# Kernel optimization log

Measured on AMD Instinct MI355X. Metric: run time of the kernel, lower is better.

Reference implementation:

```python
import jax, jax.numpy as jnp
import numpy as np

N_TOKENS = 32768
DIM = 4096
N_EXPERTS = 64
TOPK = 2
UPDATE_BIAS_RATE = 0.001
ROUTE_SCALE = 1.0


def setup_inputs() -> dict:
    key = jax.random.key(0)
    k1, k2 = jax.random.split(key)
    x = jax.random.normal(k1, (N_TOKENS, DIM), dtype=jnp.float32)
    # gate projection weight, as in nn.Parameter(torch.empty(E, dim)) + kaiming init
    weight = jax.random.normal(k2, (N_EXPERTS, DIM), dtype=jnp.float32) * 0.02
    bias = jnp.zeros((N_EXPERTS,), dtype=jnp.float32)          # registered buffer
    target_dist = jnp.full((N_EXPERTS,), 1.0 / N_EXPERTS, dtype=jnp.float32)
    return {"x": x, "weight": weight, "bias": bias, "target_dist": target_dist}


def reference(x, weight, bias, target_dist):
    # scores = linear(nan_to_num(x), W) + bias, softmax in fp32
    xc = jnp.nan_to_num(x, nan=0.0)
    scores = (xc @ weight.T + bias).astype(jnp.float32)        # [N, E]
    probs = jax.nn.softmax(scores, axis=-1)                    # [N, E]
    # top-k: gathered values equal the top-k probabilities
    topv, indices = jax.lax.top_k(probs, TOPK)                 # [N, K], [N, K]
    weights = topv / jnp.sum(topv, axis=-1, keepdims=True)
    weights = weights * ROUTE_SCALE
    # load-balancing stats: bincount with float weights == segment_sum
    expert_weights_sum = jax.ops.segment_sum(
        weights.reshape(-1), indices.reshape(-1), num_segments=N_EXPERTS)
    total_weights = expert_weights_sum.sum()
    load_error = target_dist * total_weights - expert_weights_sum
    new_bias = bias + UPDATE_BIAS_RATE * (load_error / total_weights)
    return weights.astype(x.dtype), indices, new_bias
```

## Files before the change

### kernel.cpp

```cpp
#include <hip/hip_runtime.h>
#include <math.h>

#define N_TOKENS 32768
#define DIM      4096
#define NE       64
#define TM       64
#define BK       128
#define KHALF    (DIM / 2)
#define NBLK_MAIN (N_TOKENS / TM * 2)
#define NBLK_POST (N_TOKENS / 256)
#define EPS_GAP  2e-3f
#define REFINE_BLOCKS 1024

#define WOFF     65664
#define WL_OFF   16384
#define PART_OFF 128
#define PSC_OFF  524288
#define WFRAG_ELEMS (512 * 512)

typedef __bf16 bf16x4 __attribute__((ext_vector_type(4)));
typedef __bf16 bf16x8 __attribute__((ext_vector_type(8)));
typedef float  f32x16 __attribute__((ext_vector_type(16)));

__global__ __launch_bounds__(256) void prep_w(
    const float* __restrict__ w, float* __restrict__ ws)
{
    __bf16* whi = (__bf16*)(ws + WOFF);
    __bf16* wlo = whi + WFRAG_ELEMS;
    const int tid  = blockIdx.x * 256 + threadIdx.x;
    const int f    = tid >> 6, lane = tid & 63;
    const int nt   = f & 1,    K16  = f >> 1;
    const int e    = nt * 32 + (lane & 31);
    const int k    = K16 * 16 + (lane >> 5) * 8;
    const float4 a = *(const float4*)(w + (size_t)e * DIM + k);
    const float4 b = *(const float4*)(w + (size_t)e * DIM + k + 4);
    const float v[8] = {a.x, a.y, a.z, a.w, b.x, b.y, b.z, b.w};
    bf16x8 h, l;
    #pragma unroll
    for (int i = 0; i < 8; ++i) {
        h[i] = (__bf16)v[i];
        l[i] = (__bf16)(v[i] - (float)h[i]);
    }
    *(bf16x8*)(whi + (size_t)tid * 8) = h;
    *(bf16x8*)(wlo + (size_t)tid * 8) = l;
}

__device__ __forceinline__ void cvt_split(const float4 v, bf16x4& h, bf16x4& l) {
    h[0] = (__bf16)v.x; l[0] = (__bf16)(v.x - (float)h[0]);
    h[1] = (__bf16)v.y; l[1] = (__bf16)(v.y - (float)h[1]);
    h[2] = (__bf16)v.z; l[2] = (__bf16)(v.z - (float)h[2]);
    h[3] = (__bf16)v.w; l[3] = (__bf16)(v.w - (float)h[3]);
}

__global__ __launch_bounds__(256, 4) void gate_main(
    const float* __restrict__ x,
    float* __restrict__ ws)
{
    __shared__ __align__(16) unsigned char smem[32768];

    const __bf16* whi = (const __bf16*)(ws + WOFF);
    const __bf16* wlo = whi + WFRAG_ELEMS;
    float*        psc = ws + PSC_OFF;

    const int t    = threadIdx.x;
    const int lane = t & 63;
    const int wave = t >> 6;
    const int mt   = wave >> 1;
    const int nt   = wave & 1;
    const int kh   = blockIdx.x & 1;
    const int tb   = (blockIdx.x >> 1) * TM;
    const int kbeg = kh * KHALF;

    const int q     = t & 31;
    const int rbase = t >> 5;

    f32x16 acc0, acc12;
    #pragma unroll
    for (int i = 0; i < 16; ++i) { acc0[i] = 0.f; acc12[i] = 0.f; }

    float4 xv[8];
    #pragma unroll
    for (int j = 0; j < 8; ++j)
        xv[j] = *(const float4*)(x + (size_t)(tb + rbase + 8 * j) * DIM + kbeg + q * 4);

    const int tok0  = mt * 32 + (lane & 31);
    const int klane = lane >> 5;
    const int abase = tok0 * 256;
    const int aswz  = (tok0 & 7) << 4;

    for (int kc = kbeg; kc < kbeg + KHALF; kc += BK) {
        #pragma unroll
        for (int j = 0; j < 8; ++j) {
            const int r = rbase + 8 * j;
            bf16x4 h, l;
            cvt_split(xv[j], h, l);
            const int off = r * 256 + ((q * 8) ^ ((r & 7) << 4));
            *(bf16x4*)(&smem[off])         = h;
            *(bf16x4*)(&smem[16384 + off]) = l;
        }
        __syncthreads();

        if (kc + BK < kbeg + KHALF) {
            #pragma unroll
            for (int j = 0; j < 8; ++j)
                xv[j] = *(const float4*)(x + (size_t)(tb + rbase + 8 * j) * DIM + kc + BK + q * 4);
        }

        const int K16c = kc >> 4;
        #pragma unroll
        for (int ks = 0; ks < 8; ++ks) {
            const int aoff = abase + ((ks * 32 + klane * 16) ^ aswz);
            const bf16x8 ah = *(const bf16x8*)(&smem[aoff]);
            const bf16x8 al = *(const bf16x8*)(&smem[16384 + aoff]);
            const size_t bidx = ((size_t)((K16c + ks) * 2 + nt) * 64 + lane) * 8;
            const bf16x8 bh = *(const bf16x8*)(whi + bidx);
            const bf16x8 bl = *(const bf16x8*)(wlo + bidx);
            acc0  = __builtin_amdgcn_mfma_f32_32x32x16_bf16(ah, bh, acc0,  0, 0, 0);
            acc12 = __builtin_amdgcn_mfma_f32_32x32x16_bf16(al, bh, acc12, 0, 0, 0);
            acc12 = __builtin_amdgcn_mfma_f32_32x32x16_bf16(ah, bl, acc12, 0, 0, 0);
        }
        __syncthreads();
    }

    const int e = nt * 32 + (lane & 31);
    float* base = psc + (size_t)kh * N_TOKENS * NE;
    #pragma unroll
    for (int r = 0; r < 16; ++r) {
        const int tok = mt * 32 + (r & 3) + 8 * (r >> 2) + 4 * (lane >> 5);
        base[(size_t)(tb + tok) * NE + e] = acc0[r] + acc12[r];
    }
}

__global__ __launch_bounds__(256) void gate_post(
    const float* __restrict__ bias,
    float* __restrict__ out,
    float* __restrict__ ws)
{
    __shared__ float sbias[NE];
    __shared__ float part[NE];
    unsigned* wl_count = (unsigned*)(ws + 64);
    float*    partials = ws + PART_OFF;
    int*      wl       = (int*)(ws + WL_OFF);
    const float* psc   = ws + PSC_OFF;

    const int t = threadIdx.x;
    if (t < NE) { sbias[t] = bias[t]; part[t] = 0.f; }
    __syncthreads();

    const int tok = blockIdx.x * 256 + t;
    const float* p0 = psc + (size_t)tok * NE;
    const float* p1 = psc + (size_t)N_TOKENS * NE + (size_t)tok * NE;

    float v1 = -3e38f, v2 = -3e38f, v3 = -3e38f;
    int   i1 = 0,      i2 = 0;
    #pragma unroll
    for (int g = 0; g < 16; ++g) {
        const float4 a = *(const float4*)(p0 + g * 4);
        const float4 b = *(const float4*)(p1 + g * 4);
        float s[4] = {a.x + b.x, a.y + b.y, a.z + b.z, a.w + b.w};
        #pragma unroll
        for (int j = 0; j < 4; ++j) {
            const float sv = s[j] + sbias[g * 4 + j];
            const int   e  = g * 4 + j;
            if (sv > v1)      { v3 = v2; v2 = v1; i2 = i1; v1 = sv; i1 = e; }
            else if (sv > v2) { v3 = v2; v2 = sv; i2 = e; }
            else if (sv > v3) { v3 = sv; }
        }
    }
    const bool risky = (v1 - v2 < EPS_GAP) || (v2 - v3 < EPS_GAP);
    if (risky) {
        const int pos = (int)atomicAdd(wl_count, 1u);
        wl[pos] = tok;
    } else {
        const float ex = expf(v2 - v1);
        const float w1 = 1.f / (1.f + ex);
        const float w2 = ex * w1;
        const size_t g = (size_t)tok * 2;
        *(float2*)(out + g)                        = make_float2(w1, w2);
        *(float2*)(out + (size_t)N_TOKENS * 2 + g) = make_float2((float)i1, (float)i2);
        atomicAdd(&part[i1], w1);
        atomicAdd(&part[i2], w2);
    }
    __syncthreads();
    if (t < NE) partials[(size_t)blockIdx.x * NE + t] = part[t];
}

__global__ __launch_bounds__(256) void gate_refine(
    const float* __restrict__ x,
    const float* __restrict__ w,
    const float* __restrict__ bias,
    float* __restrict__ out,
    float* __restrict__ ws)
{
    float*          ews_ref  = ws;
    const unsigned* wl_count = (const unsigned*)(ws + 64);
    const int*      wl       = (const int*)(ws + WL_OFF);

    const int t = threadIdx.x;
    const int e = t >> 2;
    const int q = t & 3;
    __shared__ double sc[NE];

    const unsigned count = *wl_count;
    for (unsigned it = blockIdx.x; it < count; it += gridDim.x) {
        const int tok = wl[it];
        const float* xr = x + (size_t)tok * DIM;
        const float* wr = w + (size_t)e * DIM;
        double s = 0.0;
        const int k0 = q * (DIM / 4), k1 = k0 + DIM / 4;
        for (int k = k0; k < k1; k += 4) {
            const float4 a = *(const float4*)(xr + k);
            const float4 b = *(const float4*)(wr + k);
            s += (double)a.x * (double)b.x;
            s += (double)a.y * (double)b.y;
            s += (double)a.z * (double)b.z;
            s += (double)a.w * (double)b.w;
        }
        s += __shfl_xor(s, 1);
        s += __shfl_xor(s, 2);
        if (q == 0) sc[e] = s + (double)bias[e];
        __syncthreads();

        if (t == 0) {
            double v1 = -1e300, v2 = -1e300;
            int i1 = 0, i2 = 0;
            for (int j = 0; j < NE; ++j) {
                const double sv = sc[j];
                if (sv > v1)      { v2 = v1; i2 = i1; v1 = sv; i1 = j; }
                else if (sv > v2) { v2 = sv; i2 = j; }
            }
            const double ex = exp(v2 - v1);
            const double w1 = 1.0 / (1.0 + ex);
            const double w2 = ex * w1;
            const size_t g = (size_t)tok * 2;
            *(float2*)(out + g)                        = make_float2((float)w1, (float)w2);
            *(float2*)(out + (size_t)N_TOKENS * 2 + g) = make_float2((float)i1, (float)i2);
            atomicAdd(&ews_ref[i1], (float)w1);
            atomicAdd(&ews_ref[i2], (float)w2);
        }
        __syncthreads();
    }
}

__global__ void gate_bias(
    const float* __restrict__ bias,
    const float* __restrict__ target,
    const float* __restrict__ ws,
    float* __restrict__ out)
{
    const int e = threadIdx.x;
    const float* partials = ws + PART_OFF;
    float v = ws[e];
    for (int b = 0; b < NBLK_POST; ++b) v += partials[(size_t)b * NE + e];
    float total = v;
    #pragma unroll
    for (int off = 32; off > 0; off >>= 1)
        total += __shfl_xor(total, off);
    const float nb = bias[e] + 0.001f * ((target[e] * total - v) / total);
    out[(size_t)N_TOKENS * 4 + e] = nb;
}

extern "C" void kernel_launch(void* const* d_in, const int* in_sizes, int n_in,
                              void* d_out, int out_size, void* d_ws, size_t ws_size,
                              hipStream_t stream) {
    const float* x      = (const float*)d_in[0];
    const float* w      = (const float*)d_in[1];
    const float* bias   = (const float*)d_in[2];
    const float* target = (const float*)d_in[3];
    float* out = (float*)d_out;
    float* ws  = (float*)d_ws;

    hipMemsetAsync(ws, 0, 128 * sizeof(float), stream);
    prep_w     <<<128, 256, 0, stream>>>(w, ws);
    gate_main  <<<NBLK_MAIN, 256, 0, stream>>>(x, ws);
    gate_post  <<<NBLK_POST, 256, 0, stream>>>(bias, out, ws);
    gate_refine<<<REFINE_BLOCKS, 256, 0, stream>>>(x, w, bias, out, ws);
    gate_bias  <<<1, 64, 0, stream>>>(bias, target, ws, out);
}
```

Measured before the change: 281.4 us.

## Restructure gate GEMM into per-wave K-quarter split without LDS staging

The main gate kernel now gives each wave a quarter of the K dimension for a 32-token tile and loads x straight into registers, dropping the shared-memory staging and both barriers. The fp32 to bf16 hi/lo split is done with bit masking (truncation) instead of rounding conversions, and B fragments are double-buffered in registers. Partial scores are written as four K-quarter planes that the post kernel now sums, which doubles partial-score traffic. Each wave covers all 64 experts, so the x hi/lo fragments are reused across two accumulators, but register pressure rises and truncation slightly changes the split error.

```diff
diff --git a/kernel.cpp b/kernel.cpp
--- a/kernel.cpp
+++ b/kernel.cpp
@@ -4,10 +4,9 @@
 #define N_TOKENS 32768
 #define DIM      4096
 #define NE       64
-#define TM       64
-#define BK       128
-#define KHALF    (DIM / 2)
-#define NBLK_MAIN (N_TOKENS / TM * 2)
+#define KQ       4
+#define KSPAN    (DIM / KQ)
+#define NBLK_MAIN (N_TOKENS / 32)
 #define NBLK_POST (N_TOKENS / 256)
 #define EPS_GAP  2e-3f
 #define REFINE_BLOCKS 1024
@@ -18,7 +17,6 @@
 #define PSC_OFF  524288
 #define WFRAG_ELEMS (512 * 512)
 
-typedef __bf16 bf16x4 __attribute__((ext_vector_type(4)));
 typedef __bf16 bf16x8 __attribute__((ext_vector_type(8)));
 typedef float  f32x16 __attribute__((ext_vector_type(16)));
 
@@ -35,99 +33,134 @@
     const float4 a = *(const float4*)(w + (size_t)e * DIM + k);
     const float4 b = *(const float4*)(w + (size_t)e * DIM + k + 4);
     const float v[8] = {a.x, a.y, a.z, a.w, b.x, b.y, b.z, b.w};
-    bf16x8 h, l;
+    __bf16 h[8], l[8];
     #pragma unroll
     for (int i = 0; i < 8; ++i) {
         h[i] = (__bf16)v[i];
         l[i] = (__bf16)(v[i] - (float)h[i]);
     }
-    *(bf16x8*)(whi + (size_t)tid * 8) = h;
-    *(bf16x8*)(wlo + (size_t)tid * 8) = l;
-}
-
-__device__ __forceinline__ void cvt_split(const float4 v, bf16x4& h, bf16x4& l) {
-    h[0] = (__bf16)v.x; l[0] = (__bf16)(v.x - (float)h[0]);
-    h[1] = (__bf16)v.y; l[1] = (__bf16)(v.y - (float)h[1]);
-    h[2] = (__bf16)v.z; l[2] = (__bf16)(v.z - (float)h[2]);
-    h[3] = (__bf16)v.w; l[3] = (__bf16)(v.w - (float)h[3]);
-}
-
-__global__ __launch_bounds__(256, 4) void gate_main(
-    const float* __restrict__ x,
-    float* __restrict__ ws)
-{
-    __shared__ __align__(16) unsigned char smem[32768];
-
+    *(bf16x8*)(whi + (size_t)tid * 8) = *(bf16x8*)h;
+    *(bf16x8*)(wlo + (size_t)tid * 8) = *(bf16x8*)l;
+}
+
+__device__ __forceinline__ unsigned pack_pair(float f0, float f1, float& r0, float& r1) {
+    const unsigned u0 = __float_as_uint(f0), u1 = __float_as_uint(f1);
+    const unsigned h0 = u0 & 0xFFFF0000u,   h1 = u1 & 0xFFFF0000u;
+    r0 = f0 - __uint_as_float(h0);
+    r1 = f1 - __uint_as_float(h1);
+    return (u0 >> 16) | h1;
+}
+__device__ __forceinline__ void cvt8(const float4 a, const float4 b, uint4& h, uint4& l) {
+    float r0, r1, r2, r3, r4, r5, r6, r7;
+    h.x = pack_pair(a.x, a.y, r0, r1);
+    h.y = pack_pair(a.z, a.w, r2, r3);
+    h.z = pack_pair(b.x, b.y, r4, r5);
+    h.w = pack_pair(b.z, b.w, r6, r7);
+    l.x = (__float_as_uint(r0) >> 16) | (__float_as_uint(r1) & 0xFFFF0000u);
+    l.y = (__float_as_uint(r2) >> 16) | (__float_as_uint(r3) & 0xFFFF0000u);
+    l.z = (__float_as_uint(r4) >> 16) | (__float_as_uint(r5) & 0xFFFF0000u);
+    l.w = (__float_as_uint(r6) >> 16) | (__float_as_uint(r7) & 0xFFFF0000u);
+}
+
+struct Bset { bf16x8 h[2][2]; bf16x8 l[2][2]; };
+
+__device__ __forceinline__ void loadB(Bset& B, const __bf16* whi, const __bf16* wlo,
+                                      int k16, int lane) {
+    #pragma unroll
+    for (int s = 0; s < 2; ++s)
+        #pragma unroll
+        for (int nt = 0; nt < 2; ++nt) {
+            const size_t idx = ((size_t)((k16 + s) * 2 + nt) * 64 + lane) * 8;
+            B.h[s][nt] = *(const bf16x8*)(whi + idx);
+            B.l[s][nt] = *(const bf16x8*)(wlo + idx);
+        }
+}
+
+__device__ __forceinline__ void mma_k32(const uint4 h0, const uint4 l0,
+                                        const uint4 h1, const uint4 l1,
+                                        const Bset& B, f32x16& acc0, f32x16& acc1) {
+    const bf16x8 ah0 = __builtin_bit_cast(bf16x8, h0);
+    const bf16x8 al0 = __builtin_bit_cast(bf16x8, l0);
+    const bf16x8 ah1 = __builtin_bit_cast(bf16x8, h1);
+    const bf16x8 al1 = __builtin_bit_cast(bf16x8, l1);
+    acc0 = __builtin_amdgcn_mfma_f32_32x32x16_bf16(ah0, B.h[0][0], acc0, 0, 0, 0);
+    acc1 = __builtin_amdgcn_mfma_f32_32x32x16_bf16(ah0, B.h[0][1], acc1, 0, 0, 0);
+    acc0 = __builtin_amdgcn_mfma_f32_32x32x16_bf16(al0, B.h[0][0], acc0, 0, 0, 0);
+    acc1 = __builtin_amdgcn_mfma_f32_32x32x16_bf16(al0, B.h[0][1], acc1, 0, 0, 0);
+    acc0 = __builtin_amdgcn_mfma_f32_32x32x16_bf16(ah0, B.l[0][0], acc0, 0, 0, 0);
+    acc1 = __builtin_amdgcn_mfma_f32_32x32x16_bf16(ah0, B.l[0][1], acc1, 0, 0, 0);
+    acc0 = __builtin_amdgcn_mfma_f32_32x32x16_bf16(ah1, B.h[1][0], acc0, 0, 0, 0);
+    acc1 = __builtin_amdgcn_mfma_f32_32x32x16_bf16(ah1, B.h[1][1], acc1, 0, 0, 0);
+    acc0 = __builtin_amdgcn_mfma_f32_32x32x16_bf16(al1, B.h[1][0], acc0, 0, 0, 0);
+    acc1 = __builtin_amdgcn_mfma_f32_32x32x16_bf16(al1, B.h[1][1], acc1, 0, 0, 0);
+    acc0 = __builtin_amdgcn_mfma_f32_32x32x16_bf16(ah1, B.l[1][0], acc0, 0, 0, 0);
+    acc1 = __builtin_amdgcn_mfma_f32_32x32x16_bf16(ah1, B.l[1][1], acc1, 0, 0, 0);
+}
+
+__global__ __launch_bounds__(256) void gate_main(
+    const float* __restrict__ x, float* __restrict__ ws)
+{
     const __bf16* whi = (const __bf16*)(ws + WOFF);
     const __bf16* wlo = whi + WFRAG_ELEMS;
     float*        psc = ws + PSC_OFF;
 
     const int t    = threadIdx.x;
     const int lane = t & 63;
-    const int wave = t >> 6;
-    const int mt   = wave >> 1;
-    const int nt   = wave & 1;
-    const int kh   = blockIdx.x & 1;
-    const int tb   = (blockIdx.x >> 1) * TM;
-    const int kbeg = kh * KHALF;
-
-    const int q     = t & 31;
-    const int rbase = t >> 5;
-
-    f32x16 acc0, acc12;
-    #pragma unroll
-    for (int i = 0; i < 16; ++i) { acc0[i] = 0.f; acc12[i] = 0.f; }
-
-    float4 xv[8];
-    #pragma unroll
-    for (int j = 0; j < 8; ++j)
-        xv[j] = *(const float4*)(x + (size_t)(tb + rbase + 8 * j) * DIM + kbeg + q * 4);
-
-    const int tok0  = mt * 32 + (lane & 31);
-    const int klane = lane >> 5;
-    const int abase = tok0 * 256;
-    const int aswz  = (tok0 & 7) << 4;
-
-    for (int kc = kbeg; kc < kbeg + KHALF; kc += BK) {
-        #pragma unroll
-        for (int j = 0; j < 8; ++j) {
-            const int r = rbase + 8 * j;
-            bf16x4 h, l;
-            cvt_split(xv[j], h, l);
-            const int off = r * 256 + ((q * 8) ^ ((r & 7) << 4));
-            *(bf16x4*)(&smem[off])         = h;
-            *(bf16x4*)(&smem[16384 + off]) = l;
-        }
-        __syncthreads();
-
-        if (kc + BK < kbeg + KHALF) {
-            #pragma unroll
-            for (int j = 0; j < 8; ++j)
-                xv[j] = *(const float4*)(x + (size_t)(tb + rbase + 8 * j) * DIM + kc + BK + q * 4);
-        }
-
-        const int K16c = kc >> 4;
-        #pragma unroll
-        for (int ks = 0; ks < 8; ++ks) {
-            const int aoff = abase + ((ks * 32 + klane * 16) ^ aswz);
-            const bf16x8 ah = *(const bf16x8*)(&smem[aoff]);
-            const bf16x8 al = *(const bf16x8*)(&smem[16384 + aoff]);
-            const size_t bidx = ((size_t)((K16c + ks) * 2 + nt) * 64 + lane) * 8;
-            const bf16x8 bh = *(const bf16x8*)(whi + bidx);
-            const bf16x8 bl = *(const bf16x8*)(wlo + bidx);
-            acc0  = __builtin_amdgcn_mfma_f32_32x32x16_bf16(ah, bh, acc0,  0, 0, 0);
-            acc12 = __builtin_amdgcn_mfma_f32_32x32x16_bf16(al, bh, acc12, 0, 0, 0);
-            acc12 = __builtin_amdgcn_mfma_f32_32x32x16_bf16(ah, bl, acc12, 0, 0, 0);
-        }
-        __syncthreads();
-    }
-
-    const int e = nt * 32 + (lane & 31);
-    float* base = psc + (size_t)kh * N_TOKENS * NE;
+    const int wv   = t >> 6;
+    const int tb   = blockIdx.x * 32;
+    const int kbeg = wv * KSPAN;
+    const int kend = kbeg + KSPAN;
+
+    const int row = tb + (lane & 31);
+    const int kh8 = (lane >> 5) * 8;
+    const float* xr = x + (size_t)row * DIM;
+
+    f32x16 acc0, acc1;
+    #pragma unroll
+    for (int i = 0; i < 16; ++i) { acc0[i] = 0.f; acc1[i] = 0.f; }
+
+    float4 xA0, xA1, xA2, xA3, xB0, xB1, xB2, xB3;
+    Bset BA, BB;
+    uint4 h0, l0, h1, l1;
+
+    #define LOADX(P0, P1, P2, P3, kc)                         \
+        P0 = *(const float4*)(xr + (kc) + kh8);               \
+        P1 = *(const float4*)(xr + (kc) + kh8 + 4);           \
+        P2 = *(const float4*)(xr + (kc) + 16 + kh8);          \
+        P3 = *(const float4*)(xr + (kc) + 16 + kh8 + 4);
+
+    LOADX(xA0, xA1, xA2, xA3, kbeg);
+    loadB(BA, whi, wlo, kbeg >> 4, lane);
+    LOADX(xB0, xB1, xB2, xB3, kbeg + 32);
+
+    for (int s = 0; s < KSPAN / 64; ++s) {
+        const int kc = kbeg + s * 64;
+
+        loadB(BB, whi, wlo, (kc + 32) >> 4, lane);
+        cvt8(xA0, xA1, h0, l0);
+        cvt8(xA2, xA3, h1, l1);
+        { const int kn = (kc + 64 < kend) ? kc + 64 : kbeg;
+          LOADX(xA0, xA1, xA2, xA3, kn); }
+        mma_k32(h0, l0, h1, l1, BA, acc0, acc1);
+
+        { const int k16n = (kc + 64 < kend) ? (kc + 64) >> 4 : kbeg >> 4;
+          loadB(BA, whi, wlo, k16n, lane); }
+        cvt8(xB0, xB1, h0, l0);
+        cvt8(xB2, xB3, h1, l1);
+        { const int kn = (kc + 96 < kend) ? kc + 96 : kbeg;
+          LOADX(xB0, xB1, xB2, xB3, kn); }
+        mma_k32(h0, l0, h1, l1, BB, acc0, acc1);
+    }
+    #undef LOADX
+
+    const int e0 = lane & 31;
+    const int rsel = 4 * (lane >> 5);
+    float* p = psc + ((size_t)wv * N_TOKENS + tb) * NE;
     #pragma unroll
     for (int r = 0; r < 16; ++r) {
-        const int tok = mt * 32 + (r & 3) + 8 * (r >> 2) + 4 * (lane >> 5);
-        base[(size_t)(tb + tok) * NE + e] = acc0[r] + acc12[r];
+        const int tok = (r & 3) + 8 * (r >> 2) + rsel;
+        p[(size_t)tok * NE + e0]      = acc0[r];
+        p[(size_t)tok * NE + e0 + 32] = acc1[r];
     }
 }
 
@@ -142,25 +175,28 @@
     float*    partials = ws + PART_OFF;
     int*      wl       = (int*)(ws + WL_OFF);
     const float* psc   = ws + PSC_OFF;
+    const size_t PL    = (size_t)N_TOKENS * NE;
 
     const int t = threadIdx.x;
     if (t < NE) { sbias[t] = bias[t]; part[t] = 0.f; }
     __syncthreads();
 
     const int tok = blockIdx.x * 256 + t;
-    const float* p0 = psc + (size_t)tok * NE;
-    const float* p1 = psc + (size_t)N_TOKENS * NE + (size_t)tok * NE;
+    const float* p = psc + (size_t)tok * NE;
 
     float v1 = -3e38f, v2 = -3e38f, v3 = -3e38f;
     int   i1 = 0,      i2 = 0;
     #pragma unroll
     for (int g = 0; g < 16; ++g) {
-        const float4 a = *(const float4*)(p0 + g * 4);
-        const float4 b = *(const float4*)(p1 + g * 4);
-        float s[4] = {a.x + b.x, a.y + b.y, a.z + b.z, a.w + b.w};
+        const float4 a = *(const float4*)(p + g * 4);
+        const float4 b = *(const float4*)(p + PL + g * 4);
+        const float4 c = *(const float4*)(p + 2 * PL + g * 4);
+        const float4 d = *(const float4*)(p + 3 * PL + g * 4);
+        float sv4[4] = {(a.x + b.x) + (c.x + d.x), (a.y + b.y) + (c.y + d.y),
+                        (a.z + b.z) + (c.z + d.z), (a.w + b.w) + (c.w + d.w)};
         #pragma unroll
         for (int j = 0; j < 4; ++j) {
-            const float sv = s[j] + sbias[g * 4 + j];
+            const float sv = sv4[j] + sbias[g * 4 + j];
             const int   e  = g * 4 + j;
             if (sv > v1)      { v3 = v2; v2 = v1; i2 = i1; v1 = sv; i1 = e; }
             else if (sv > v2) { v3 = v2; v2 = sv; i2 = e; }
```

Result: slower. 330.8 us (+17.6%).

## Load x tiles straight into LDS as fp32 and split to bf16 at MFMA read

Applied to the files above, without the earlier changes.

The gate GEMM no longer stages x through registers and converts it to hi/lo bf16 before writing LDS. Instead, global_load_lds writes raw fp32 x into a swizzled LDS tile, and each wave converts its MFMA operands at read time using a bit-mask truncation split instead of round-to-nearest. The aim is to cut register pressure and the VALU convert/store traffic in the load phase, and launch_bounds drops the min-blocks hint. The trade-off is a lost register prefetch of the next tile, no overlap between load and compute, conversion work redone by both n-tile waves, and truncation instead of rounding for the hi part.

```diff
diff --git a/kernel.cpp b/kernel.cpp
--- a/kernel.cpp
+++ b/kernel.cpp
@@ -18,7 +18,6 @@
 #define PSC_OFF  524288
 #define WFRAG_ELEMS (512 * 512)
 
-typedef __bf16 bf16x4 __attribute__((ext_vector_type(4)));
 typedef __bf16 bf16x8 __attribute__((ext_vector_type(8)));
 typedef float  f32x16 __attribute__((ext_vector_type(16)));
 
@@ -35,28 +34,45 @@
     const float4 a = *(const float4*)(w + (size_t)e * DIM + k);
     const float4 b = *(const float4*)(w + (size_t)e * DIM + k + 4);
     const float v[8] = {a.x, a.y, a.z, a.w, b.x, b.y, b.z, b.w};
-    bf16x8 h, l;
+    __bf16 h[8], l[8];
     #pragma unroll
     for (int i = 0; i < 8; ++i) {
         h[i] = (__bf16)v[i];
         l[i] = (__bf16)(v[i] - (float)h[i]);
     }
-    *(bf16x8*)(whi + (size_t)tid * 8) = h;
-    *(bf16x8*)(wlo + (size_t)tid * 8) = l;
-}
-
-__device__ __forceinline__ void cvt_split(const float4 v, bf16x4& h, bf16x4& l) {
-    h[0] = (__bf16)v.x; l[0] = (__bf16)(v.x - (float)h[0]);
-    h[1] = (__bf16)v.y; l[1] = (__bf16)(v.y - (float)h[1]);
-    h[2] = (__bf16)v.z; l[2] = (__bf16)(v.z - (float)h[2]);
-    h[3] = (__bf16)v.w; l[3] = (__bf16)(v.w - (float)h[3]);
-}
-
-__global__ __launch_bounds__(256, 4) void gate_main(
-    const float* __restrict__ x,
-    float* __restrict__ ws)
-{
-    __shared__ __align__(16) unsigned char smem[32768];
+    *(bf16x8*)(whi + (size_t)tid * 8) = *(bf16x8*)h;
+    *(bf16x8*)(wlo + (size_t)tid * 8) = *(bf16x8*)l;
+}
+
+__device__ __forceinline__ unsigned pack_pair(float f0, float f1, float& r0, float& r1) {
+    const unsigned u0 = __float_as_uint(f0), u1 = __float_as_uint(f1);
+    const unsigned h0 = u0 & 0xFFFF0000u,   h1 = u1 & 0xFFFF0000u;
+    r0 = f0 - __uint_as_float(h0);
+    r1 = f1 - __uint_as_float(h1);
+    return (u0 >> 16) | h1;
+}
+__device__ __forceinline__ void cvt8(const float4 a, const float4 b, uint4& h, uint4& l) {
+    float r0, r1, r2, r3, r4, r5, r6, r7;
+    h.x = pack_pair(a.x, a.y, r0, r1);
+    h.y = pack_pair(a.z, a.w, r2, r3);
+    h.z = pack_pair(b.x, b.y, r4, r5);
+    h.w = pack_pair(b.z, b.w, r6, r7);
+    l.x = (__float_as_uint(r0) >> 16) | (__float_as_uint(r1) & 0xFFFF0000u);
+    l.y = (__float_as_uint(r2) >> 16) | (__float_as_uint(r3) & 0xFFFF0000u);
+    l.z = (__float_as_uint(r4) >> 16) | (__float_as_uint(r5) & 0xFFFF0000u);
+    l.w = (__float_as_uint(r6) >> 16) | (__float_as_uint(r7) & 0xFFFF0000u);
+}
+
+__device__ __forceinline__ void gload_lds16(const float* g, float* lds) {
+    __builtin_amdgcn_global_load_lds(
+        (const __attribute__((address_space(1))) unsigned*)g,
+        (__attribute__((address_space(3))) unsigned*)lds, 16, 0, 0);
+}
+
+__global__ __launch_bounds__(256) void gate_main(
+    const float* __restrict__ x, float* __restrict__ ws)
+{
+    __shared__ __align__(16) float xs[TM * BK];
 
     const __bf16* whi = (const __bf16*)(ws + WOFF);
     const __bf16* wlo = whi + WFRAG_ELEMS;
@@ -71,50 +87,41 @@
     const int tb   = (blockIdx.x >> 1) * TM;
     const int kbeg = kh * KHALF;
 
-    const int q     = t & 31;
-    const int rbase = t >> 5;
+    const int l31 = lane & 31, lhi = lane >> 5;
+
+    size_t sbase[8];
+    #pragma unroll
+    for (int wl = 0; wl < 8; ++wl) {
+        const int row = wave * 16 + wl * 2 + lhi;
+        const int col = l31 ^ (row & 31);
+        sbase[wl] = (size_t)(tb + row) * DIM + kbeg + col * 4;
+    }
+
+    const int a_row = mt * 32 + l31;
 
     f32x16 acc0, acc12;
     #pragma unroll
     for (int i = 0; i < 16; ++i) { acc0[i] = 0.f; acc12[i] = 0.f; }
 
-    float4 xv[8];
-    #pragma unroll
-    for (int j = 0; j < 8; ++j)
-        xv[j] = *(const float4*)(x + (size_t)(tb + rbase + 8 * j) * DIM + kbeg + q * 4);
-
-    const int tok0  = mt * 32 + (lane & 31);
-    const int klane = lane >> 5;
-    const int abase = tok0 * 256;
-    const int aswz  = (tok0 & 7) << 4;
-
-    for (int kc = kbeg; kc < kbeg + KHALF; kc += BK) {
+    for (int s = 0; s < KHALF / BK; ++s) {
         #pragma unroll
-        for (int j = 0; j < 8; ++j) {
-            const int r = rbase + 8 * j;
-            bf16x4 h, l;
-            cvt_split(xv[j], h, l);
-            const int off = r * 256 + ((q * 8) ^ ((r & 7) << 4));
-            *(bf16x4*)(&smem[off])         = h;
-            *(bf16x4*)(&smem[16384 + off]) = l;
-        }
-        __syncthreads();
-
-        if (kc + BK < kbeg + KHALF) {
-            #pragma unroll
-            for (int j = 0; j < 8; ++j)
-                xv[j] = *(const float4*)(x + (size_t)(tb + rbase + 8 * j) * DIM + kc + BK + q * 4);
-        }
-
-        const int K16c = kc >> 4;
+        for (int wl = 0; wl < 8; ++wl)
+            gload_lds16(x + sbase[wl] + s * BK, &xs[(wave * 16 + wl * 2) * BK]);
+        __syncthreads();
+
+        const int K16c = (kbeg + s * BK) >> 4;
         #pragma unroll
         for (int ks = 0; ks < 8; ++ks) {
-            const int aoff = abase + ((ks * 32 + klane * 16) ^ aswz);
-            const bf16x8 ah = *(const bf16x8*)(&smem[aoff]);
-            const bf16x8 al = *(const bf16x8*)(&smem[16384 + aoff]);
+            const int s0 = ks * 4 + (lhi << 1);
+            const float4 fa = *(const float4*)&xs[a_row * BK + ((s0 ^ l31) << 2)];
+            const float4 fb = *(const float4*)&xs[a_row * BK + (((s0 + 1) ^ l31) << 2)];
+            uint4 h, l;
+            cvt8(fa, fb, h, l);
             const size_t bidx = ((size_t)((K16c + ks) * 2 + nt) * 64 + lane) * 8;
             const bf16x8 bh = *(const bf16x8*)(whi + bidx);
             const bf16x8 bl = *(const bf16x8*)(wlo + bidx);
+            const bf16x8 ah = __builtin_bit_cast(bf16x8, h);
+            const bf16x8 al = __builtin_bit_cast(bf16x8, l);
             acc0  = __builtin_amdgcn_mfma_f32_32x32x16_bf16(ah, bh, acc0,  0, 0, 0);
             acc12 = __builtin_amdgcn_mfma_f32_32x32x16_bf16(al, bh, acc12, 0, 0, 0);
             acc12 = __builtin_amdgcn_mfma_f32_32x32x16_bf16(ah, bl, acc12, 0, 0, 0);
@@ -122,12 +129,11 @@
         __syncthreads();
     }
 
-    const int e = nt * 32 + (lane & 31);
-    float* base = psc + (size_t)kh * N_TOKENS * NE;
+    float* p = psc + (size_t)kh * N_TOKENS * NE + (size_t)tb * NE;
     #pragma unroll
     for (int r = 0; r < 16; ++r) {
-        const int tok = mt * 32 + (r & 3) + 8 * (r >> 2) + 4 * (lane >> 5);
-        base[(size_t)(tb + tok) * NE + e] = acc0[r] + acc12[r];
+        const int tok = mt * 32 + (r & 3) + 8 * (r >> 2) + 4 * lhi;
+        p[(size_t)tok * NE + nt * 32 + l31] = acc0[r] + acc12[r];
     }
 }
 
@@ -142,25 +148,25 @@
     float*    partials = ws + PART_OFF;
     int*      wl       = (int*)(ws + WL_OFF);
     const float* psc   = ws + PSC_OFF;
+    const size_t PL    = (size_t)N_TOKENS * NE;
 
     const int t = threadIdx.x;
     if (t < NE) { sbias[t] = bias[t]; part[t] = 0.f; }
     __syncthreads();
 
     const int tok = blockIdx.x * 256 + t;
-    const float* p0 = psc + (size_t)tok * NE;
-    const float* p1 = psc + (size_t)N_TOKENS * NE + (size_t)tok * NE;
+    const float* p = psc + (size_t)tok * NE;
 
     float v1 = -3e38f, v2 = -3e38f, v3 = -3e38f;
     int   i1 = 0,      i2 = 0;
     #pragma unroll
     for (int g = 0; g < 16; ++g) {
-        const float4 a = *(const float4*)(p0 + g * 4);
-        const float4 b = *(const float4*)(p1 + g * 4);
-        float s[4] = {a.x + b.x, a.y + b.y, a.z + b.z, a.w + b.w};
+        const float4 a = *(const float4*)(p + g * 4);
+        const float4 b = *(const float4*)(p + PL + g * 4);
+        float sv4[4] = {a.x + b.x, a.y + b.y, a.z + b.z, a.w + b.w};
         #pragma unroll
         for (int j = 0; j < 4; ++j) {
-            const float sv = s[j] + sbias[g * 4 + j];
+            const float sv = sv4[j] + sbias[g * 4 + j];
             const int   e  = g * 4 + j;
             if (sv > v1)      { v3 = v2; v2 = v1; i2 = i1; v1 = sv; i1 = e; }
             else if (sv > v2) { v3 = v2; v2 = sv; i2 = e; }
```

New measurement: 298.1 us. 5.9% more time.
